# Optimization experiments

Measured on AMD Instinct MI355X. Metric: run time of the kernel, lower is better.

Reference implementation:

```python
import jax, jax.numpy as jnp
import numpy as np

B, T = 256, 50
N_ITEMS = 100000
EMB = 256      # embedding
KBD = 128      # KBembedding == MN_dims
HID = 256      # layers[0] == layers[-1]
OUT = 256      # out_dim
NF = 10        # MN_nfactors == n_r


def setup_inputs() -> dict:
    key = jax.random.key(0)
    ks = jax.random.split(key, 18)
    s = 0.05
    return {
        "X": jax.random.randint(ks[0], (B, T), 0, N_ITEMS),
        "E": jax.random.normal(ks[1], (N_ITEMS, EMB), jnp.float32) * s,
        "KBE": jax.random.normal(ks[2], (N_ITEMS, KBD), jnp.float32) * s,
        "r_matrix": jax.random.normal(ks[3], (NF, KBD), jnp.float32) * s,
        "W_ih": jax.random.normal(ks[4], (3 * HID, EMB), jnp.float32) * s,
        "W_hh": jax.random.normal(ks[5], (3 * HID, HID), jnp.float32) * s,
        "b_ih": jnp.zeros((3 * HID,), jnp.float32),
        "b_hh": jnp.zeros((3 * HID,), jnp.float32),
        "MNu_W": jax.random.normal(ks[6], (KBD, HID), jnp.float32) * s,
        "MNu_b": jnp.zeros((KBD,), jnp.float32),
        "MNu2_W": jax.random.normal(ks[7], (HID, KBD + HID), jnp.float32) * s,
        "MNu2_b": jnp.zeros((HID,), jnp.float32),
        "MNea_W": jax.random.normal(ks[8], (KBD, KBD), jnp.float32) * s,
        "MNea_b": jnp.zeros((KBD,), jnp.float32),
        "mlp1_W": jax.random.normal(ks[9], (OUT, HID), jnp.float32) * s,
        "mlp1_b": jnp.zeros((OUT,), jnp.float32),
        "mlp2_W": jax.random.normal(ks[10], (OUT, EMB + KBD), jnp.float32) * s,
        "mlp2_b": jnp.zeros((OUT,), jnp.float32),
    }


def _gru_cell(x, h, W_ih, W_hh, b_ih, b_hh):
    # PyTorch GRUCell: gates stacked [r, z, n] along dim 0 of weights
    gi = x @ W_ih.T + b_ih
    gh = h @ W_hh.T + b_hh
    ir, iz, inn = jnp.split(gi, 3, axis=-1)
    hr, hz, hn = jnp.split(gh, 3, axis=-1)
    r = jax.nn.sigmoid(ir + hr)
    z = jax.nn.sigmoid(iz + hz)
    n = jnp.tanh(inn + r * hn)
    return (1.0 - z) * n + z * h


def reference(X, E, KBE, r_matrix, W_ih, W_hh, b_ih, b_hh,
              MNu_W, MNu_b, MNu2_W, MNu2_b, MNea_W, MNea_b,
              mlp1_W, mlp1_b, mlp2_W, mlp2_b):
    Bv, Tv = X.shape
    Em = E.at[0].set(0.0)     # mask row 0 of E
    KBm = KBE.at[0].set(0.0)  # mask row 0 of KBE
    Sx = Em[X]                # (B, T, EMB)
    KBItem = KBm[X]           # (B, T, KBD)

    def step(carry, xs):
        h, MN, y_sum = carry
        x_t, kb_t = xs                      # (B, EMB), (B, KBD)
        h = _gru_cell(x_t, h, W_ih, W_hh, b_ih, b_hh)
        y = h                                # dropout p=0 -> identity
        # gated memory write
        EA = jnp.tanh(kb_t @ MNea_W.T + MNea_b)          # (B, KBD)
        EA = EA[:, None, :] + r_matrix                    # (B, NF, KBD)
        gate = jax.nn.sigmoid(jnp.sum(MN * EA, axis=-1, keepdims=True))  # (B, NF, 1)
        MN = MN * (1.0 - gate) + EA * gate
        # attention read
        U = jnp.tanh(y @ MNu_W.T + MNu_b)                 # (B, KBD)
        AW = jax.nn.softmax(U @ r_matrix.T, axis=1)       # (B, NF)
        AC = jnp.einsum('bfd,bf->bd', MN, AW)             # (B, KBD)
        Ut = jnp.tanh(jnp.concatenate([y, AC], axis=-1) @ MNu2_W.T + MNu2_b)  # (B, HID)
        y_out = jnp.tanh(Ut @ mlp1_W.T + mlp1_b)          # (B, OUT)
        return (h, MN, y_sum + y_out), None

    init = (jnp.zeros((Bv, HID), Sx.dtype),
            jnp.zeros((Bv, NF, KBD), Sx.dtype),
            jnp.zeros((Bv, OUT), Sx.dtype))
    xs = (jnp.swapaxes(Sx, 0, 1), jnp.swapaxes(KBItem, 0, 1))  # (T, B, *)
    (h, MN, y_sum), _ = jax.lax.scan(step, init, xs)
    y = y_sum / Tv

    MergeE = jnp.concatenate([E, KBE], axis=1).at[0].set(0.0)  # (N, EMB+KBD)
    Sy = jnp.tanh(MergeE @ mlp2_W.T + mlp2_b)                  # (N, OUT)
    scores = jax.nn.log_softmax(y @ Sy.T, axis=1)              # (B, N)
    return scores, y
```

## Files before the change

kernel.cpp:

```cpp
#include <hip/hip_runtime.h>

typedef _Float16 f16;
typedef _Float16 f16x4 __attribute__((ext_vector_type(4)));
typedef _Float16 f16x8 __attribute__((ext_vector_type(8)));
typedef float f32x4 __attribute__((ext_vector_type(4)));

#define MFMA16(a,b,c) __builtin_amdgcn_mfma_f32_16x16x32_f16(a,b,c,0,0,0)

#define NITEMS 100000
#define NBLK4  1563

#define OFF_WIH   0u
#define OFF_WHH   393216u
#define OFF_MNU   786432u
#define OFF_MNU2  851968u
#define OFF_MNEA  1048576u
#define OFF_MLP1  1081344u
#define OFF_MLP2  1212416u
#define OFF_GI    1409024u
#define OFF_TV    21069824u
#define OFF_MN    24346624u
#define OFF_YALL  57114624u
#define OFF_SY    66945024u
#define OFF_Y16   118407168u
#define OFF_PMAX  118538240u
#define OFF_PSUM  120176640u
#define OFF_LSE   121815040u

__device__ __forceinline__ float sigm(float x) { return 1.f / (1.f + __expf(-x)); }
__device__ __forceinline__ float tanh_fast(float x) {
  return 1.f - 2.f / (1.f + __expf(2.f * x));
}

__global__ __launch_bounds__(256) void k_pack(
    const float* s0, const float* s1, const float* s2, const float* s3,
    const float* s4, const float* s5, const float* s6, f16* base)
{
  int fid = blockIdx.x * 256 + threadIdx.x;
  const float* src; f16* dst; int K, f;
  if (fid < 24576)      { src = s0; dst = base;          K = 256; f = fid; }
  else if (fid < 49152) { src = s1; dst = base + 196608; K = 256; f = fid - 24576; }
  else if (fid < 53248) { src = s2; dst = base + 393216; K = 256; f = fid - 49152; }
  else if (fid < 65536) { src = s3; dst = base + 425984; K = 384; f = fid - 53248; }
  else if (fid < 67584) { src = s4; dst = base + 524288; K = 128; f = fid - 65536; }
  else if (fid < 75776) { src = s5; dst = base + 540672; K = 256; f = fid - 67584; }
  else                  { src = s6; dst = base + 606208; K = 384; f = fid - 75776; }
  int lane = f & 63, t2 = f >> 6, KS = K >> 5;
  int ks = t2 % KS, nt = t2 / KS;
  int row = nt * 16 + (lane & 15), col = ks * 32 + ((lane >> 4) << 3);
  const float* sp = src + (size_t)row * K + col;
  f16x8 v;
  #pragma unroll
  for (int j = 0; j < 8; j++) v[j] = (f16)sp[j];
  *(f16x8*)(dst + (size_t)f * 8) = v;
}

__global__ __launch_bounds__(512) void k_giea(
    const int* __restrict__ X, const float* __restrict__ E,
    const f16* __restrict__ Wih_p, const float* __restrict__ bih,
    const float* __restrict__ bhh, f16* __restrict__ gi2,
    const float* __restrict__ KBE, const f16* __restrict__ Wea_p,
    const float* __restrict__ bea, f16* __restrict__ tv)
{
  __shared__ __align__(16) char smem[66048];
  f16 (*At)[264] = (f16(*)[264])smem;
  f16* Lg2 = (f16*)(smem + 16896);
  int tid = threadIdx.x;
  int w = tid >> 6, lane = tid & 63, lr = lane & 15, lg = lane >> 4;
  if (blockIdx.x < 400) {
    int r0g = blockIdx.x * 32;
    int t = r0g >> 8;
    int grp0 = (r0g & 255) >> 3;
    {
      int r = tid >> 4, c = (tid & 15) * 16;
      int b = (r0g + r) & 255;
      int item = X[b * 50 + t];
      if (item == 0) {
        #pragma unroll
        for (int j = 0; j < 16; j++) At[r][c + j] = (f16)0.f;
      } else {
        const float4* sp = (const float4*)(E + (size_t)item * 256 + c);
        #pragma unroll
        for (int q = 0; q < 4; q++) {
          float4 v = sp[q];
          At[r][c + q*4 + 0] = (f16)v.x; At[r][c + q*4 + 1] = (f16)v.y;
          At[r][c + q*4 + 2] = (f16)v.z; At[r][c + q*4 + 3] = (f16)v.w;
        }
      }
    }
    __syncthreads();
    f32x4 acc[2][6] = {};
    for (int ks = 0; ks < 8; ks++) {
      f16x8 a0 = *(const f16x8*)(&At[lr][ks * 32 + lg * 8]);
      f16x8 a1 = *(const f16x8*)(&At[16 + lr][ks * 32 + lg * 8]);
      #pragma unroll
      for (int j = 0; j < 6; j++) {
        int nt = w * 6 + j;
        f16x8 bf = *(const f16x8*)(Wih_p + ((size_t)((nt * 8 + ks) * 64 + lane) << 3));
        acc[0][j] = MFMA16(a0, bf, acc[0][j]);
        acc[1][j] = MFMA16(a1, bf, acc[1][j]);
      }
    }
    int lane_s = ((lg & 1) << 4) | lr;
    #pragma unroll
    for (int j = 0; j < 6; j++) {
      int tile = w * 6 + j;
      int gate = tile >> 4, w_s = tile & 15;
      int col = tile * 16 + lr;
      float bias = bih[col] + (col < 512 ? bhh[col] : 0.f);
      #pragma unroll
      for (int mt = 0; mt < 2; mt++) {
        int grp_local = mt * 2 + (lg >> 1);
        f16* dstp = Lg2 + (((grp_local * 16 + w_s) * 32 + lane_s) * 12 + gate * 4);
        #pragma unroll
        for (int rr = 0; rr < 4; rr++)
          dstp[rr] = (f16)(acc[mt][j][rr] + bias);
      }
    }
    __syncthreads();
    f16* dst = gi2 + ((size_t)t * 32 + grp0) * 6144;
    #pragma unroll
    for (int q = 0; q < 6; q++) {
      int i = q * 512 + tid;
      *(f16x8*)(dst + i * 8) = *(const f16x8*)(Lg2 + i * 8);
    }
  } else {
    int r0 = (blockIdx.x - 400) * 32;
    int t = r0 >> 8;
    {
      int r = tid >> 4, c = (tid & 15) * 8;
      int b = (r0 + r) & 255;
      int item = X[b * 50 + t];
      if (item == 0) {
        #pragma unroll
        for (int j = 0; j < 8; j++) At[r][c + j] = (f16)0.f;
      } else {
        const float4* sp = (const float4*)(KBE + (size_t)item * 128 + c);
        #pragma unroll
        for (int q = 0; q < 2; q++) {
          float4 v = sp[q];
          At[r][c + q*4 + 0] = (f16)v.x; At[r][c + q*4 + 1] = (f16)v.y;
          At[r][c + q*4 + 2] = (f16)v.z; At[r][c + q*4 + 3] = (f16)v.w;
        }
      }
    }
    __syncthreads();
    f32x4 acc[2] = {};
    for (int ks = 0; ks < 4; ks++) {
      f16x8 a0 = *(const f16x8*)(&At[lr][ks * 32 + lg * 8]);
      f16x8 a1 = *(const f16x8*)(&At[16 + lr][ks * 32 + lg * 8]);
      f16x8 bf = *(const f16x8*)(Wea_p + ((size_t)((w * 4 + ks) * 64 + lane) << 3));
      acc[0] = MFMA16(a0, bf, acc[0]);
      acc[1] = MFMA16(a1, bf, acc[1]);
    }
    f16* tvs = Lg2;
    int col = w * 16 + lr;
    float bias = bea[col];
    #pragma unroll
    for (int mt = 0; mt < 2; mt++)
      #pragma unroll
      for (int rr = 0; rr < 4; rr++)
        tvs[(mt * 16 + lg * 4 + rr) * 128 + col] = (f16)tanh_fast(acc[mt][rr] + bias);
    __syncthreads();
    {
      int row = tid >> 4, c = (tid & 15) * 8;
      *(f16x8*)(tv + (size_t)(r0 + row) * 128 + c) = *(const f16x8*)(tvs + row * 128 + c);
    }
  }
}

__global__ __launch_bounds__(1024)
__attribute__((amdgpu_waves_per_eu(4, 4)))
void k_fused(
    const f16* __restrict__ Whh_p, const float* __restrict__ bhh,
    const f16* __restrict__ gi2, f16* __restrict__ y_all,
    const f16* __restrict__ tv, const float* __restrict__ Rm, f16* __restrict__ MN,
    const float* __restrict__ E, const float* __restrict__ KBE,
    const f16* __restrict__ mlp2_p, const float* __restrict__ mlp2b, f16* __restrict__ Sy)
{
  __shared__ __align__(16) char smem[147456];
  int tid = threadIdx.x, w = tid >> 6, lane = tid & 63, lr = lane & 15, lg = lane >> 4;

  if (blockIdx.x < 32) {
    f16* Wlds = (f16*)smem;
    f16* hb0 = (f16*)(smem + 131072);
    f16* hb1 = (f16*)(smem + 139264);
    int r0 = blockIdx.x * 8;
    {
      const float4* src = (const float4*)Whh_p;
      float4* dst = (float4*)Wlds;
      #pragma unroll
      for (int i = 0; i < 8; i++) dst[tid + i * 1024] = src[tid + i * 1024];
      float4 z4 = {0.f, 0.f, 0.f, 0.f};
      ((float4*)hb0)[tid] = z4;
    }
    int col = w * 16 + lr;
    float bN = bhh[col + 512];
    float hreg[4] = {0.f, 0.f, 0.f, 0.f};
    const f16* gP = gi2 + (size_t)blockIdx.x * 6144 + (size_t)(w * 32 + lane) * 12;
    f16x8 P0 = {};
    f16x4 P1 = {};
    if (lg < 2) {
      P0 = *(const f16x8*)gP;
      P1 = *(const f16x4*)(gP + 8);
    }
    __syncthreads();
    f16* hc = hb0; f16* hn_ = hb1;
    int xr = (lr & 7) << 4;
    const f16* wB0 = Wlds + (size_t)w * 4096 + lane * 8;
    const f16* wBz = Whh_p + ((size_t)((16 + w) * 8) * 64 + lane) * 8;
    const f16* wBn = Whh_p + ((size_t)((32 + w) * 8) * 64 + lane) * 8;
    for (int t = 0; t < 50; t++) {
      f32x4 aR = {}, aZ = {}, aN = {};
      const char* hbase = (const char*)hc + lr * 512;
      #pragma unroll
      for (int ks = 0; ks < 8; ks++) {
        f16x8 a = *(const f16x8*)(hbase + ((ks * 64 + lg * 16) ^ xr));
        aR = MFMA16(a, *(const f16x8*)(wB0 + ks * 512), aR);
        aZ = MFMA16(a, *(const f16x8*)(wBz + ks * 512), aZ);
        aN = MFMA16(a, *(const f16x8*)(wBn + ks * 512), aN);
      }
      if (lg < 2) {
        #pragma unroll
        for (int rr = 0; rr < 4; rr++) {
          int row = lg * 4 + rr;
          float rg = sigm((float)P0[rr] + aR[rr]);
          float zg = sigm((float)P0[4 + rr] + aZ[rr]);
          float ng = tanh_fast((float)P1[rr] + rg * (aN[rr] + bN));
          float hv = ng + zg * (hreg[rr] - ng);
          hreg[rr] = hv;
          *(f16*)((char*)hn_ + row * 512 + ((col * 2) ^ ((row & 7) << 4))) = (f16)hv;
        }
        if (t < 49) {
          const f16* gN = gP + (size_t)(t + 1) * 196608;
          P0 = *(const f16x8*)gN;
          P1 = *(const f16x4*)(gN + 8);
        }
      }
      __syncthreads();
      if (tid < 256) {
        int row = tid >> 5, c = tid & 31;
        f16x8 hv = *(const f16x8*)((char*)hn_ + row * 512 + ((c * 16) ^ ((row & 7) << 4)));
        *(f16x8*)(y_all + ((size_t)t * 256 + r0 + row) * 256 + c * 8) = hv;
      }
      f16* tmp = hc; hc = hn_; hn_ = tmp;
    }
  } else if (blockIdx.x < 192) {
    int pair = (blockIdx.x - 32) * 16 + w;
    int b = pair / 10, f = pair - (pair / 10) * 10;
    float r0_ = Rm[f * 128 + lane], r1_ = Rm[f * 128 + 64 + lane];
    float mn0 = 0.f, mn1 = 0.f;
    float c0 = (float)tv[(size_t)b * 128 + lane];
    float c1 = (float)tv[(size_t)b * 128 + 64 + lane];
    for (int t = 0; t < 50; t++) {
      float ea0 = c0 + r0_;
      float ea1 = c1 + r1_;
      if (t < 49) {
        size_t nb = ((size_t)(t + 1) * 256 + b) * 128;
        c0 = (float)tv[nb + lane];
        c1 = (float)tv[nb + 64 + lane];
      }
      float p = mn0 * ea0 + mn1 * ea1;
      #pragma unroll
      for (int off = 32; off > 0; off >>= 1) p += __shfl_xor(p, off);
      float g = sigm(p);
      mn0 += (ea0 - mn0) * g;
      mn1 += (ea1 - mn1) * g;
      size_t mb = (((size_t)t * 256 + b) * 10 + f) * 128;
      MN[mb + lane] = (f16)mn0;
      MN[mb + 64 + lane] = (f16)mn1;
    }
  } else {
    f16* At = (f16*)smem;
    int i0 = (blockIdx.x - 192) * 32;
    {
      int r = tid >> 5;
      int item = i0 + r;
      int c = (tid & 31) * 8;
      if (item == 0) {
        #pragma unroll
        for (int j = 0; j < 8; j++) At[r * 392 + c + j] = (f16)0.f;
      } else {
        const float4* sp = (const float4*)(E + (size_t)item * 256 + c);
        #pragma unroll
        for (int q = 0; q < 2; q++) {
          float4 v = sp[q];
          At[r * 392 + c + q*4 + 0] = (f16)v.x; At[r * 392 + c + q*4 + 1] = (f16)v.y;
          At[r * 392 + c + q*4 + 2] = (f16)v.z; At[r * 392 + c + q*4 + 3] = (f16)v.w;
        }
      }
      int c2 = (tid & 31) * 4;
      if (item == 0) {
        #pragma unroll
        for (int j = 0; j < 4; j++) At[r * 392 + 256 + c2 + j] = (f16)0.f;
      } else {
        float4 v = *(const float4*)(KBE + (size_t)item * 128 + c2);
        At[r * 392 + 256 + c2 + 0] = (f16)v.x; At[r * 392 + 256 + c2 + 1] = (f16)v.y;
        At[r * 392 + 256 + c2 + 2] = (f16)v.z; At[r * 392 + 256 + c2 + 3] = (f16)v.w;
      }
    }
    __syncthreads();
    int mt = w & 1, ntp = w >> 1;
    f32x4 acc[2] = {};
    for (int ks = 0; ks < 12; ks++) {
      f16x8 a = *(const f16x8*)(&At[(mt * 16 + lr) * 392 + ks * 32 + lg * 8]);
      #pragma unroll
      for (int j = 0; j < 2; j++) {
        int nt = ntp * 2 + j;
        f16x8 bf = *(const f16x8*)(mlp2_p + ((size_t)((nt * 12 + ks) * 64 + lane) << 3));
        acc[j] = MFMA16(a, bf, acc[j]);
      }
    }
    #pragma unroll
    for (int j = 0; j < 2; j++) {
      int col = (ntp * 2 + j) * 16 + lr;
      float bias = mlp2b[col];
      #pragma unroll
      for (int rr = 0; rr < 4; rr++) {
        int item = i0 + mt * 16 + lg * 4 + rr;
        Sy[(size_t)item * 256 + col] = (f16)tanh_fast(acc[j][rr] + bias);
      }
    }
  }
}

__global__ __launch_bounds__(512) void k_uacut(
    const f16* __restrict__ y_all, const f16* __restrict__ MNu_p,
    const float* __restrict__ MNub, const float* __restrict__ Rm,
    const f16* __restrict__ MN,
    const f16* __restrict__ MNu2_p, const float* __restrict__ MNu2b,
    const f16* __restrict__ mlp1_p, const float* __restrict__ mlp1b,
    float* __restrict__ ypart)
{
  __shared__ __align__(16) char smem[25088];
  int tid = threadIdx.x, w = tid >> 6, lane = tid & 63, lr = lane & 15, lg = lane >> 4;
  f16   (*Aty)[264] = (f16(*)[264])smem;
  float (*Uf)[136]  = (float(*)[136])(smem + 8448);
  f16   (*Utl)[264] = (f16(*)[264])(smem + 8448);
  float (*Lg)[10]   = (float(*)[10])(smem + 17152);
  float (*Aw)[10]   = (float(*)[10])(smem + 17792);
  f16   (*ACs)[136] = (f16(*)[136])(smem + 18432);
  int r0 = blockIdx.x * 16;
  {
    int r = tid >> 5, c = (tid & 31) * 8;
    f16x8 v = *(const f16x8*)(y_all + (size_t)(r0 + r) * 256 + c);
    *(f16x8*)(&Aty[r][c]) = v;
  }
  __syncthreads();
  {
    f32x4 acc = {};
    for (int ks = 0; ks < 8; ks++) {
      f16x8 a = *(const f16x8*)(&Aty[lr][ks * 32 + lg * 8]);
      f16x8 bf = *(const f16x8*)(MNu_p + ((size_t)((w * 8 + ks) * 64 + lane) << 3));
      acc = MFMA16(a, bf, acc);
    }
    int col = w * 16 + lr;
    float bias = MNub[col];
    #pragma unroll
    for (int rr = 0; rr < 4; rr++)
      Uf[lg * 4 + rr][col] = tanh_fast(acc[rr] + bias);
  }
  __syncthreads();
  if (tid < 160) {
    int row = tid / 10, f = tid - (tid / 10) * 10;
    float s = 0.f;
    for (int d = 0; d < 128; d++) s += Uf[row][d] * Rm[f * 128 + d];
    Lg[row][f] = s;
  }
  __syncthreads();
  if (tid < 16) {
    float m = -1e30f;
    #pragma unroll
    for (int f = 0; f < 10; f++) m = fmaxf(m, Lg[tid][f]);
    float e[10], s = 0.f;
    #pragma unroll
    for (int f = 0; f < 10; f++) { e[f] = __expf(Lg[tid][f] - m); s += e[f]; }
    float inv = 1.f / s;
    #pragma unroll
    for (int f = 0; f < 10; f++) Aw[tid][f] = e[f] * inv;
  }
  __syncthreads();
  if (tid < 256) {
    int row = tid >> 4, d0 = (tid & 15) * 8;
    float a[8] = {0,0,0,0,0,0,0,0};
    for (int f = 0; f < 10; f++) {
      float wgt = Aw[row][f];
      f16x8 mv = *(const f16x8*)(MN + (((size_t)(r0 + row)) * 10 + f) * 128 + d0);
      #pragma unroll
      for (int q = 0; q < 8; q++) a[q] += wgt * (float)mv[q];
    }
    f16x8 o;
    #pragma unroll
    for (int q = 0; q < 8; q++) o[q] = (f16)a[q];
    *(f16x8*)(&ACs[row][d0]) = o;
  }
  __syncthreads();
  {
    f32x4 acc[2] = {};
    for (int ks = 0; ks < 12; ks++) {
      f16x8 a = (ks < 8)
        ? *(const f16x8*)(&Aty[lr][ks * 32 + lg * 8])
        : *(const f16x8*)(&ACs[lr][(ks - 8) * 32 + lg * 8]);
      #pragma unroll
      for (int j = 0; j < 2; j++) {
        f16x8 bf = *(const f16x8*)(MNu2_p + ((size_t)(((w * 2 + j) * 12 + ks) * 64 + lane) << 3));
        acc[j] = MFMA16(a, bf, acc[j]);
      }
    }
    __syncthreads();
    #pragma unroll
    for (int j = 0; j < 2; j++) {
      int col = (w * 2 + j) * 16 + lr;
      float bias = MNu2b[col];
      #pragma unroll
      for (int rr = 0; rr < 4; rr++)
        Utl[lg * 4 + rr][col] = (f16)tanh_fast(acc[j][rr] + bias);
    }
  }
  __syncthreads();
  {
    f32x4 acc2[2] = {};
    for (int ks = 0; ks < 8; ks++) {
      f16x8 a = *(const f16x8*)(&Utl[lr][ks * 32 + lg * 8]);
      #pragma unroll
      for (int j = 0; j < 2; j++) {
        f16x8 bf = *(const f16x8*)(mlp1_p + ((size_t)(((w * 2 + j) * 8 + ks) * 64 + lane) << 3));
        acc2[j] = MFMA16(a, bf, acc2[j]);
      }
    }
    #pragma unroll
    for (int j = 0; j < 2; j++) {
      int col = (w * 2 + j) * 16 + lr;
      float bias = mlp1b[col];
      #pragma unroll
      for (int rr = 0; rr < 4; rr++) {
        int row = r0 + lg * 4 + rr;
        ypart[(size_t)row * 256 + col] = tanh_fast(acc2[j][rr] + bias);
      }
    }
  }
}

__global__ __launch_bounds__(256) void k_yfin(
    const float* __restrict__ ypart, float* __restrict__ outy, f16* __restrict__ y16)
{
  int b = blockIdx.x, c = threadIdx.x;
  float s = 0.f;
  for (int t = 0; t < 50; t++) s += ypart[((size_t)t * 256 + b) * 256 + c];
  float v = s * (1.0f / 50.0f);
  outy[b * 256 + c] = v;
  y16[b * 256 + c] = (f16)v;
}

__global__ __launch_bounds__(512) void k_score0(
    const f16* __restrict__ y16, const f16* __restrict__ Sy,
    float* __restrict__ pmax, float* __restrict__ psum)
{
  __shared__ float pm[512], ps[512];
  int tid = threadIdx.x, w = tid >> 6, lane = tid & 63, lr = lane & 15, lg = lane >> 4;
  int i0 = blockIdx.x * 64;
  int mtb = (w >> 1) * 4, ntb = (w & 1) * 2;
  f32x4 acc[4][2] = {};
  for (int ks = 0; ks < 8; ks++) {
    f16x8 a[4];
    #pragma unroll
    for (int i = 0; i < 4; i++)
      a[i] = *(const f16x8*)(y16 + ((size_t)((mtb + i) * 16 + lr)) * 256 + ks * 32 + lg * 8);
    #pragma unroll
    for (int j = 0; j < 2; j++) {
      int item = i0 + (ntb + j) * 16 + lr;
      int ic = item < NITEMS ? item : (NITEMS - 1);
      f16x8 bv = *(const f16x8*)(Sy + (size_t)ic * 256 + ks * 32 + lg * 8);
      #pragma unroll
      for (int i = 0; i < 4; i++) acc[i][j] = MFMA16(a[i], bv, acc[i][j]);
    }
  }
  {
    int item0 = i0 + ntb * 16 + lr, item1 = item0 + 16;
    bool v0 = item0 < NITEMS, v1 = item1 < NITEMS;
    #pragma unroll
    for (int i = 0; i < 4; i++)
      #pragma unroll
      for (int rr = 0; rr < 4; rr++) {
        float x0 = v0 ? acc[i][0][rr] : -1e30f;
        float x1 = v1 ? acc[i][1][rr] : -1e30f;
        float m = fmaxf(x0, x1);
        m = fmaxf(m, __shfl_xor(m, 1)); m = fmaxf(m, __shfl_xor(m, 2));
        m = fmaxf(m, __shfl_xor(m, 4)); m = fmaxf(m, __shfl_xor(m, 8));
        float s = (v0 ? __expf(x0 - m) : 0.f) + (v1 ? __expf(x1 - m) : 0.f);
        s += __shfl_xor(s, 1); s += __shfl_xor(s, 2);
        s += __shfl_xor(s, 4); s += __shfl_xor(s, 8);
        if (lr == 0) {
          int row = (mtb + i) * 16 + lg * 4 + rr;
          pm[(w & 1) * 256 + row] = m;
          ps[(w & 1) * 256 + row] = s;
        }
      }
  }
  __syncthreads();
  if (tid < 256) {
    float m0 = pm[tid], m1 = pm[256 + tid];
    float s0 = ps[tid], s1 = ps[256 + tid];
    float M = fmaxf(m0, m1);
    float S = s0 * __expf(m0 - M) + s1 * __expf(m1 - M);
    pmax[(size_t)tid * 1600 + blockIdx.x] = M;
    psum[(size_t)tid * 1600 + blockIdx.x] = S;
  }
}

__global__ __launch_bounds__(256) void k_lse(
    const float* __restrict__ pmax, const float* __restrict__ psum, float* __restrict__ lse)
{
  int b = blockIdx.x, tid = threadIdx.x;
  __shared__ float red[256];
  float m = -1e30f;
  for (int i = tid; i < NBLK4; i += 256) m = fmaxf(m, pmax[(size_t)b * 1600 + i]);
  red[tid] = m; __syncthreads();
  for (int s = 128; s > 0; s >>= 1) {
    if (tid < s) red[tid] = fmaxf(red[tid], red[tid + s]);
    __syncthreads();
  }
  float M = red[0]; __syncthreads();
  float s = 0.f;
  for (int i = tid; i < NBLK4; i += 256)
    s += psum[(size_t)b * 1600 + i] * __expf(pmax[(size_t)b * 1600 + i] - M);
  red[tid] = s; __syncthreads();
  for (int q = 128; q > 0; q >>= 1) {
    if (tid < q) red[tid] += red[tid + q];
    __syncthreads();
  }
  if (tid == 0) lse[b] = M + logf(red[0]);
}

__global__ __launch_bounds__(512) void k_scores1(
    const f16* __restrict__ y16, const f16* __restrict__ Sy,
    const float* __restrict__ lse, float* __restrict__ out)
{
  __shared__ float lse_s[256];
  int tid = threadIdx.x, w = tid >> 6, lane = tid & 63, lr = lane & 15, lg = lane >> 4;
  if (tid < 256) lse_s[tid] = lse[tid];
  int i0 = blockIdx.x * 64;
  int mtb = (w >> 1) * 4, ntb = (w & 1) * 2;
  f32x4 acc[4][2] = {};
  for (int ks = 0; ks < 8; ks++) {
    f16x8 a[4];
    #pragma unroll
    for (int i = 0; i < 4; i++)
      a[i] = *(const f16x8*)(y16 + ((size_t)((mtb + i) * 16 + lr)) * 256 + ks * 32 + lg * 8);
    #pragma unroll
    for (int j = 0; j < 2; j++) {
      int item = i0 + (ntb + j) * 16 + lr;
      int ic = item < NITEMS ? item : (NITEMS - 1);
      f16x8 bv = *(const f16x8*)(Sy + (size_t)ic * 256 + ks * 32 + lg * 8);
      #pragma unroll
      for (int i = 0; i < 4; i++) acc[i][j] = MFMA16(a[i], bv, acc[i][j]);
    }
  }
  __syncthreads();
  #pragma unroll
  for (int i = 0; i < 4; i++)
    #pragma unroll
    for (int j = 0; j < 2; j++) {
      int c = i0 + (ntb + j) * 16 + lr;
      if (c < NITEMS) {
        #pragma unroll
        for (int rr = 0; rr < 4; rr++) {
          int row = (mtb + i) * 16 + lg * 4 + rr;
          out[(size_t)row * NITEMS + c] = acc[i][j][rr] - lse_s[row];
        }
      }
    }
}

extern "C" void kernel_launch(void* const* d_in, const int* in_sizes, int n_in,
                              void* d_out, int out_size, void* d_ws, size_t ws_size,
                              hipStream_t stream) {
  (void)in_sizes; (void)n_in; (void)out_size; (void)ws_size;
  const int*   X     = (const int*)d_in[0];
  const float* E     = (const float*)d_in[1];
  const float* KBE   = (const float*)d_in[2];
  const float* Rm    = (const float*)d_in[3];
  const float* Wih   = (const float*)d_in[4];
  const float* Whh   = (const float*)d_in[5];
  const float* bih   = (const float*)d_in[6];
  const float* bhh   = (const float*)d_in[7];
  const float* MNuW  = (const float*)d_in[8];
  const float* MNub  = (const float*)d_in[9];
  const float* MNu2W = (const float*)d_in[10];
  const float* MNu2b = (const float*)d_in[11];
  const float* MNeaW = (const float*)d_in[12];
  const float* MNeab = (const float*)d_in[13];
  const float* mlp1W = (const float*)d_in[14];
  const float* mlp1b = (const float*)d_in[15];
  const float* mlp2W = (const float*)d_in[16];
  const float* mlp2b = (const float*)d_in[17];

  char* ws = (char*)d_ws;
  f16*   Wih_p  = (f16*)(ws + OFF_WIH);
  f16*   Whh_p  = (f16*)(ws + OFF_WHH);
  f16*   MNu_p  = (f16*)(ws + OFF_MNU);
  f16*   MNu2_p = (f16*)(ws + OFF_MNU2);
  f16*   Wea_p  = (f16*)(ws + OFF_MNEA);
  f16*   mlp1_p = (f16*)(ws + OFF_MLP1);
  f16*   mlp2_p = (f16*)(ws + OFF_MLP2);
  f16*   gi2    = (f16*)(ws + OFF_GI);
  f16*   tv     = (f16*)(ws + OFF_TV);
  f16*   MN     = (f16*)(ws + OFF_MN);
  f16*   y_all  = (f16*)(ws + OFF_YALL);
  f16*   Sy     = (f16*)(ws + OFF_SY);
  float* ypart  = (float*)(ws + OFF_GI);
  f16*   y16    = (f16*)(ws + OFF_Y16);
  float* pmax   = (float*)(ws + OFF_PMAX);
  float* psum   = (float*)(ws + OFF_PSUM);
  float* lse    = (float*)(ws + OFF_LSE);
  float* outf   = (float*)d_out;

  k_pack<<<344, 256, 0, stream>>>(Wih, Whh, MNuW, MNu2W, MNeaW, mlp1W, mlp2W, (f16*)ws);
  k_giea<<<800, 512, 0, stream>>>(X, E, Wih_p, bih, bhh, gi2, KBE, Wea_p, MNeab, tv);
  k_fused<<<3317, 1024, 0, stream>>>(Whh_p, bhh, gi2, y_all, tv, Rm, MN,
                                     E, KBE, mlp2_p, mlp2b, Sy);
  k_uacut<<<800, 512, 0, stream>>>(y_all, MNu_p, MNub, Rm, MN,
                                   MNu2_p, MNu2b, mlp1_p, mlp1b, ypart);
  k_yfin<<<256, 256, 0, stream>>>(ypart, outf + 25600000, y16);
  k_score0<<<NBLK4, 512, 0, stream>>>(y16, Sy, pmax, psum);
  k_lse<<<256, 256, 0, stream>>>(pmax, psum, lse);
  k_scores1<<<NBLK4, 512, 0, stream>>>(y16, Sy, lse, outf);
}
```

Baseline: 368.4 us.

## Run GRU scan one batch row per block with register-resident W_hh dot2

Replaces the 32-block MFMA GRU recurrence, which staged W_hh in LDS and processed 8 batch rows per block, with 256 blocks that each run one batch row. Every block keeps its slice of W_hh in registers and computes the recurrent gates with fdot2 plus cross-lane shuffles. The Sy (mlp2) projection moves out of the fused scan kernel into the prep kernel, and the gi layout becomes a plain row-major layout. The aim is to spread the serial recurrence across more CUs and shorten per-step latency, at the cost of loading W_hh once per block and heavier register use.

```diff
diff --git a/kernel.cpp b/kernel.cpp
--- a/kernel.cpp
+++ b/kernel.cpp
@@ -1,9 +1,10 @@
 #include <hip/hip_runtime.h>
 
 typedef _Float16 f16;
-typedef _Float16 f16x4 __attribute__((ext_vector_type(4)));
+typedef _Float16 f16x2 __attribute__((ext_vector_type(2)));
 typedef _Float16 f16x8 __attribute__((ext_vector_type(8)));
 typedef float f32x4 __attribute__((ext_vector_type(4)));
+typedef int i32x4 __attribute__((ext_vector_type(4)));
 
 #define MFMA16(a,b,c) __builtin_amdgcn_mfma_f32_16x16x32_f16(a,b,c,0,0,0)
 
@@ -17,26 +18,48 @@
 #define OFF_MNEA  1048576u
 #define OFF_MLP1  1081344u
 #define OFF_MLP2  1212416u
-#define OFF_GI    1409024u
-#define OFF_TV    21069824u
-#define OFF_MN    24346624u
-#define OFF_YALL  57114624u
-#define OFF_SY    66945024u
-#define OFF_Y16   118407168u
-#define OFF_PMAX  118538240u
-#define OFF_PSUM  120176640u
-#define OFF_LSE   121815040u
+#define OFF_WHHD  1409024u
+#define OFF_GI    1802240u
+#define OFF_TV    21463040u
+#define OFF_MN    24739840u
+#define OFF_YALL  57507840u
+#define OFF_SY    64061440u
+#define OFF_Y16   115261440u
+#define OFF_PMAX  115392512u
+#define OFF_PSUM  117030912u
+#define OFF_LSE   118669312u
 
 __device__ __forceinline__ float sigm(float x) { return 1.f / (1.f + __expf(-x)); }
 __device__ __forceinline__ float tanh_fast(float x) {
   return 1.f - 2.f / (1.f + __expf(2.f * x));
 }
+__device__ __forceinline__ float fdot2(f16x2 a, f16x2 b, float c) {
+#if defined(__has_builtin)
+#if __has_builtin(__builtin_amdgcn_fdot2)
+  return __builtin_amdgcn_fdot2(a, b, c, false);
+#else
+  return fmaf((float)a[1], (float)b[1], fmaf((float)a[0], (float)b[0], c));
+#endif
+#else
+  return fmaf((float)a[1], (float)b[1], fmaf((float)a[0], (float)b[0], c));
+#endif
+}
 
 __global__ __launch_bounds__(256) void k_pack(
     const float* s0, const float* s1, const float* s2, const float* s3,
     const float* s4, const float* s5, const float* s6, f16* base)
 {
   int fid = blockIdx.x * 256 + threadIdx.x;
+  if (fid >= 88064) {
+    int g = fid - 88064;
+    const float* sp = s1 + (size_t)g * 8;
+    f16* dst = (f16*)((char*)base + OFF_WHHD);
+    f16x8 v;
+    #pragma unroll
+    for (int j = 0; j < 8; j++) v[j] = (f16)sp[j];
+    *(f16x8*)(dst + (size_t)g * 8) = v;
+    return;
+  }
   const float* src; f16* dst; int K, f;
   if (fid < 24576)      { src = s0; dst = base;          K = 256; f = fid; }
   else if (fid < 49152) { src = s1; dst = base + 196608; K = 256; f = fid - 24576; }
@@ -55,12 +78,13 @@
   *(f16x8*)(dst + (size_t)f * 8) = v;
 }
 
-__global__ __launch_bounds__(512) void k_giea(
+__global__ __launch_bounds__(512) void k_prep(
     const int* __restrict__ X, const float* __restrict__ E,
     const f16* __restrict__ Wih_p, const float* __restrict__ bih,
-    const float* __restrict__ bhh, f16* __restrict__ gi2,
+    const float* __restrict__ bhh, f16* __restrict__ gi,
     const float* __restrict__ KBE, const f16* __restrict__ Wea_p,
-    const float* __restrict__ bea, f16* __restrict__ tv)
+    const float* __restrict__ bea, f16* __restrict__ tv,
+    const f16* __restrict__ mlp2_p, const float* __restrict__ mlp2b, f16* __restrict__ Sy)
 {
   __shared__ __align__(16) char smem[66048];
   f16 (*At)[264] = (f16(*)[264])smem;
@@ -70,7 +94,6 @@
   if (blockIdx.x < 400) {
     int r0g = blockIdx.x * 32;
     int t = r0g >> 8;
-    int grp0 = (r0g & 255) >> 3;
     {
       int r = tid >> 4, c = (tid & 15) * 16;
       int b = (r0g + r) & 255;
@@ -101,30 +124,24 @@
         acc[1][j] = MFMA16(a1, bf, acc[1][j]);
       }
     }
-    int lane_s = ((lg & 1) << 4) | lr;
     #pragma unroll
     for (int j = 0; j < 6; j++) {
-      int tile = w * 6 + j;
-      int gate = tile >> 4, w_s = tile & 15;
-      int col = tile * 16 + lr;
+      int col = (w * 6 + j) * 16 + lr;
       float bias = bih[col] + (col < 512 ? bhh[col] : 0.f);
       #pragma unroll
-      for (int mt = 0; mt < 2; mt++) {
-        int grp_local = mt * 2 + (lg >> 1);
-        f16* dstp = Lg2 + (((grp_local * 16 + w_s) * 32 + lane_s) * 12 + gate * 4);
+      for (int mt = 0; mt < 2; mt++)
         #pragma unroll
         for (int rr = 0; rr < 4; rr++)
-          dstp[rr] = (f16)(acc[mt][j][rr] + bias);
-      }
-    }
-    __syncthreads();
-    f16* dst = gi2 + ((size_t)t * 32 + grp0) * 6144;
+          Lg2[(mt * 16 + lg * 4 + rr) * 768 + col] = (f16)(acc[mt][j][rr] + bias);
+    }
+    __syncthreads();
+    f16* dst = gi + (size_t)r0g * 768;
     #pragma unroll
     for (int q = 0; q < 6; q++) {
-      int i = q * 512 + tid;
-      *(f16x8*)(dst + i * 8) = *(const f16x8*)(Lg2 + i * 8);
-    }
-  } else {
+      int u = q * 512 + tid;
+      *(f16x8*)(dst + u * 8) = *(const f16x8*)(Lg2 + u * 8);
+    }
+  } else if (blockIdx.x < 800) {
     int r0 = (blockIdx.x - 400) * 32;
     int t = r0 >> 8;
     {
@@ -166,87 +183,132 @@
       int row = tid >> 4, c = (tid & 15) * 8;
       *(f16x8*)(tv + (size_t)(r0 + row) * 128 + c) = *(const f16x8*)(tvs + row * 128 + c);
     }
-  }
-}
-
-__global__ __launch_bounds__(1024)
-__attribute__((amdgpu_waves_per_eu(4, 4)))
-void k_fused(
-    const f16* __restrict__ Whh_p, const float* __restrict__ bhh,
-    const f16* __restrict__ gi2, f16* __restrict__ y_all,
-    const f16* __restrict__ tv, const float* __restrict__ Rm, f16* __restrict__ MN,
-    const float* __restrict__ E, const float* __restrict__ KBE,
-    const f16* __restrict__ mlp2_p, const float* __restrict__ mlp2b, f16* __restrict__ Sy)
-{
-  __shared__ __align__(16) char smem[147456];
-  int tid = threadIdx.x, w = tid >> 6, lane = tid & 63, lr = lane & 15, lg = lane >> 4;
-
-  if (blockIdx.x < 32) {
-    f16* Wlds = (f16*)smem;
-    f16* hb0 = (f16*)(smem + 131072);
-    f16* hb1 = (f16*)(smem + 139264);
-    int r0 = blockIdx.x * 8;
+  } else {
+    f16* A2 = (f16*)smem;
+    int i0 = (blockIdx.x - 800) * 32;
     {
-      const float4* src = (const float4*)Whh_p;
-      float4* dst = (float4*)Wlds;
-      #pragma unroll
-      for (int i = 0; i < 8; i++) dst[tid + i * 1024] = src[tid + i * 1024];
-      float4 z4 = {0.f, 0.f, 0.f, 0.f};
-      ((float4*)hb0)[tid] = z4;
-    }
-    int col = w * 16 + lr;
-    float bN = bhh[col + 512];
-    float hreg[4] = {0.f, 0.f, 0.f, 0.f};
-    const f16* gP = gi2 + (size_t)blockIdx.x * 6144 + (size_t)(w * 32 + lane) * 12;
-    f16x8 P0 = {};
-    f16x4 P1 = {};
-    if (lg < 2) {
-      P0 = *(const f16x8*)gP;
-      P1 = *(const f16x4*)(gP + 8);
-    }
-    __syncthreads();
-    f16* hc = hb0; f16* hn_ = hb1;
-    int xr = (lr & 7) << 4;
-    const f16* wB0 = Wlds + (size_t)w * 4096 + lane * 8;
-    const f16* wBz = Whh_p + ((size_t)((16 + w) * 8) * 64 + lane) * 8;
-    const f16* wBn = Whh_p + ((size_t)((32 + w) * 8) * 64 + lane) * 8;
+      int r = tid >> 4;
+      int item = i0 + r;
+      f16* rowp = A2 + r * 392;
+      int cE = (tid & 15) * 16, cK = (tid & 15) * 8;
+      if (item == 0) {
+        #pragma unroll
+        for (int j = 0; j < 16; j++) rowp[cE + j] = (f16)0.f;
+        #pragma unroll
+        for (int j = 0; j < 8; j++) rowp[256 + cK + j] = (f16)0.f;
+      } else {
+        const float4* sp = (const float4*)(E + (size_t)item * 256 + cE);
+        #pragma unroll
+        for (int q = 0; q < 4; q++) {
+          float4 v = sp[q];
+          rowp[cE + q*4 + 0] = (f16)v.x; rowp[cE + q*4 + 1] = (f16)v.y;
+          rowp[cE + q*4 + 2] = (f16)v.z; rowp[cE + q*4 + 3] = (f16)v.w;
+        }
+        const float4* kp = (const float4*)(KBE + (size_t)item * 128 + cK);
+        #pragma unroll
+        for (int q = 0; q < 2; q++) {
+          float4 v = kp[q];
+          rowp[256 + cK + q*4 + 0] = (f16)v.x; rowp[256 + cK + q*4 + 1] = (f16)v.y;
+          rowp[256 + cK + q*4 + 2] = (f16)v.z; rowp[256 + cK + q*4 + 3] = (f16)v.w;
+        }
+      }
+    }
+    __syncthreads();
+    int mt = w & 1, nq = w >> 1;
+    f32x4 acc[4] = {};
+    for (int ks = 0; ks < 12; ks++) {
+      f16x8 a = *(const f16x8*)(&A2[(mt * 16 + lr) * 392 + ks * 32 + lg * 8]);
+      #pragma unroll
+      for (int j = 0; j < 4; j++) {
+        int nt = nq * 4 + j;
+        f16x8 bf = *(const f16x8*)(mlp2_p + ((size_t)((nt * 12 + ks) * 64 + lane) << 3));
+        acc[j] = MFMA16(a, bf, acc[j]);
+      }
+    }
+    #pragma unroll
+    for (int j = 0; j < 4; j++) {
+      int col = (nq * 4 + j) * 16 + lr;
+      float bias = mlp2b[col];
+      #pragma unroll
+      for (int rr = 0; rr < 4; rr++) {
+        int item = i0 + mt * 16 + lg * 4 + rr;
+        Sy[(size_t)item * 256 + col] = (f16)tanh_fast(acc[j][rr] + bias);
+      }
+    }
+  }
+}
+
+__global__ __launch_bounds__(1024) void k_scan(
+    const f16* __restrict__ Whh_d, const float* __restrict__ bhh,
+    const f16* __restrict__ gi, f16* __restrict__ y_all,
+    const f16* __restrict__ tv, const float* __restrict__ Rm, f16* __restrict__ MN)
+{
+  int tid = threadIdx.x, w = tid >> 6, l = tid & 63;
+  if (blockIdx.x < 256) {
+    __shared__ __align__(16) f16 hbuf[4 * 72];
+    __shared__ float ghbuf[768];
+    int b = blockIdx.x;
+    int chunk = l >> 4, cl = l & 15;
+    i32x4 Wv[3][8];
+    #pragma unroll
+    for (int j = 0; j < 3; j++) {
+      int col = w * 48 + j * 16 + cl;
+      const f16* wp = Whh_d + (size_t)col * 256 + chunk * 64;
+      #pragma unroll
+      for (int m = 0; m < 8; m++)
+        Wv[j][m] = *(const i32x4*)(wp + m * 8);
+    }
+    float hprev = 0.f, bN = 0.f;
+    f16 gr = (f16)0.f, gz = (f16)0.f, gn = (f16)0.f;
+    if (tid < 256) {
+      hbuf[(tid >> 6) * 72 + (tid & 63)] = (f16)0.f;
+      bN = bhh[512 + tid];
+      const f16* g0 = gi + (size_t)b * 768 + tid;
+      gr = g0[0]; gz = g0[256]; gn = g0[512];
+    }
+    __syncthreads();
+    const f16* hb = hbuf + chunk * 72;
     for (int t = 0; t < 50; t++) {
-      f32x4 aR = {}, aZ = {}, aN = {};
-      const char* hbase = (const char*)hc + lr * 512;
-      #pragma unroll
-      for (int ks = 0; ks < 8; ks++) {
-        f16x8 a = *(const f16x8*)(hbase + ((ks * 64 + lg * 16) ^ xr));
-        aR = MFMA16(a, *(const f16x8*)(wB0 + ks * 512), aR);
-        aZ = MFMA16(a, *(const f16x8*)(wBz + ks * 512), aZ);
-        aN = MFMA16(a, *(const f16x8*)(wBn + ks * 512), aN);
-      }
-      if (lg < 2) {
-        #pragma unroll
-        for (int rr = 0; rr < 4; rr++) {
-          int row = lg * 4 + rr;
-          float rg = sigm((float)P0[rr] + aR[rr]);
-          float zg = sigm((float)P0[4 + rr] + aZ[rr]);
-          float ng = tanh_fast((float)P1[rr] + rg * (aN[rr] + bN));
-          float hv = ng + zg * (hreg[rr] - ng);
-          hreg[rr] = hv;
-          *(f16*)((char*)hn_ + row * 512 + ((col * 2) ^ ((row & 7) << 4))) = (f16)hv;
-        }
-        if (t < 49) {
-          const f16* gN = gP + (size_t)(t + 1) * 196608;
-          P0 = *(const f16x8*)gN;
-          P1 = *(const f16x4*)(gN + 8);
-        }
+      float s0 = 0.f, s1 = 0.f, s2 = 0.f;
+      #pragma unroll
+      for (int m = 0; m < 8; m++) {
+        i32x4 hw = *(const i32x4*)(hb + m * 8);
+        #pragma unroll
+        for (int p = 0; p < 4; p++) {
+          f16x2 hp = __builtin_bit_cast(f16x2, hw[p]);
+          s0 = fdot2(hp, __builtin_bit_cast(f16x2, Wv[0][m][p]), s0);
+          s1 = fdot2(hp, __builtin_bit_cast(f16x2, Wv[1][m][p]), s1);
+          s2 = fdot2(hp, __builtin_bit_cast(f16x2, Wv[2][m][p]), s2);
+        }
+      }
+      s0 += __shfl_xor(s0, 16); s0 += __shfl_xor(s0, 32);
+      s1 += __shfl_xor(s1, 16); s1 += __shfl_xor(s1, 32);
+      s2 += __shfl_xor(s2, 16); s2 += __shfl_xor(s2, 32);
+      if (l < 16) {
+        ghbuf[w * 48 + l]      = s0;
+        ghbuf[w * 48 + 16 + l] = s1;
+        ghbuf[w * 48 + 32 + l] = s2;
       }
       __syncthreads();
       if (tid < 256) {
-        int row = tid >> 5, c = tid & 31;
-        f16x8 hv = *(const f16x8*)((char*)hn_ + row * 512 + ((c * 16) ^ ((row & 7) << 4)));
-        *(f16x8*)(y_all + ((size_t)t * 256 + r0 + row) * 256 + c * 8) = hv;
-      }
-      f16* tmp = hc; hc = hn_; hn_ = tmp;
-    }
-  } else if (blockIdx.x < 192) {
-    int pair = (blockIdx.x - 32) * 16 + w;
+        int c = tid;
+        float rg = sigm((float)gr + ghbuf[c]);
+        float zg = sigm((float)gz + ghbuf[256 + c]);
+        float ng = tanh_fast((float)gn + rg * (ghbuf[512 + c] + bN));
+        float hv = ng + zg * (hprev - ng);
+        hprev = hv;
+        hbuf[(c >> 6) * 72 + (c & 63)] = (f16)hv;
+        y_all[((size_t)t * 256 + b) * 256 + c] = (f16)hv;
+        if (t < 49) {
+          const f16* gN = gi + ((size_t)(t + 1) * 256 + b) * 768 + c;
+          gr = gN[0]; gz = gN[256]; gn = gN[512];
+        }
+      }
+      __syncthreads();
+    }
+  } else {
+    int lane = l;
+    int pair = (blockIdx.x - 256) * 16 + w;
     int b = pair / 10, f = pair - (pair / 10) * 10;
     float r0_ = Rm[f * 128 + lane], r1_ = Rm[f * 128 + 64 + lane];
     float mn0 = 0.f, mn1 = 0.f;
@@ -269,57 +331,6 @@
       size_t mb = (((size_t)t * 256 + b) * 10 + f) * 128;
       MN[mb + lane] = (f16)mn0;
       MN[mb + 64 + lane] = (f16)mn1;
-    }
-  } else {
-    f16* At = (f16*)smem;
-    int i0 = (blockIdx.x - 192) * 32;
-    {
-      int r = tid >> 5;
-      int item = i0 + r;
-      int c = (tid & 31) * 8;
-      if (item == 0) {
-        #pragma unroll
-        for (int j = 0; j < 8; j++) At[r * 392 + c + j] = (f16)0.f;
-      } else {
-        const float4* sp = (const float4*)(E + (size_t)item * 256 + c);
-        #pragma unroll
-        for (int q = 0; q < 2; q++) {
-          float4 v = sp[q];
-          At[r * 392 + c + q*4 + 0] = (f16)v.x; At[r * 392 + c + q*4 + 1] = (f16)v.y;
-          At[r * 392 + c + q*4 + 2] = (f16)v.z; At[r * 392 + c + q*4 + 3] = (f16)v.w;
-        }
-      }
-      int c2 = (tid & 31) * 4;
-      if (item == 0) {
-        #pragma unroll
-        for (int j = 0; j < 4; j++) At[r * 392 + 256 + c2 + j] = (f16)0.f;
-      } else {
-        float4 v = *(const float4*)(KBE + (size_t)item * 128 + c2);
-        At[r * 392 + 256 + c2 + 0] = (f16)v.x; At[r * 392 + 256 + c2 + 1] = (f16)v.y;
-        At[r * 392 + 256 + c2 + 2] = (f16)v.z; At[r * 392 + 256 + c2 + 3] = (f16)v.w;
-      }
-    }
-    __syncthreads();
-    int mt = w & 1, ntp = w >> 1;
-    f32x4 acc[2] = {};
-    for (int ks = 0; ks < 12; ks++) {
-      f16x8 a = *(const f16x8*)(&At[(mt * 16 + lr) * 392 + ks * 32 + lg * 8]);
-      #pragma unroll
-      for (int j = 0; j < 2; j++) {
-        int nt = ntp * 2 + j;
-        f16x8 bf = *(const f16x8*)(mlp2_p + ((size_t)((nt * 12 + ks) * 64 + lane) << 3));
-        acc[j] = MFMA16(a, bf, acc[j]);
-      }
-    }
-    #pragma unroll
-    for (int j = 0; j < 2; j++) {
-      int col = (ntp * 2 + j) * 16 + lr;
-      float bias = mlp2b[col];
-      #pragma unroll
-      for (int rr = 0; rr < 4; rr++) {
-        int item = i0 + mt * 16 + lg * 4 + rr;
-        Sy[(size_t)item * 256 + col] = (f16)tanh_fast(acc[j][rr] + bias);
-      }
     }
   }
 }
@@ -597,13 +608,13 @@
 
   char* ws = (char*)d_ws;
   f16*   Wih_p  = (f16*)(ws + OFF_WIH);
-  f16*   Whh_p  = (f16*)(ws + OFF_WHH);
   f16*   MNu_p  = (f16*)(ws + OFF_MNU);
   f16*   MNu2_p = (f16*)(ws + OFF_MNU2);
   f16*   Wea_p  = (f16*)(ws + OFF_MNEA);
   f16*   mlp1_p = (f16*)(ws + OFF_MLP1);
   f16*   mlp2_p = (f16*)(ws + OFF_MLP2);
-  f16*   gi2    = (f16*)(ws + OFF_GI);
+  f16*   Whh_d  = (f16*)(ws + OFF_WHHD);
+  f16*   gi     = (f16*)(ws + OFF_GI);
   f16*   tv     = (f16*)(ws + OFF_TV);
   f16*   MN     = (f16*)(ws + OFF_MN);
   f16*   y_all  = (f16*)(ws + OFF_YALL);
@@ -615,10 +626,10 @@
   float* lse    = (float*)(ws + OFF_LSE);
   float* outf   = (float*)d_out;
 
-  k_pack<<<344, 256, 0, stream>>>(Wih, Whh, MNuW, MNu2W, MNeaW, mlp1W, mlp2W, (f16*)ws);
-  k_giea<<<800, 512, 0, stream>>>(X, E, Wih_p, bih, bhh, gi2, KBE, Wea_p, MNeab, tv);
-  k_fused<<<3317, 1024, 0, stream>>>(Whh_p, bhh, gi2, y_all, tv, Rm, MN,
-                                     E, KBE, mlp2_p, mlp2b, Sy);
+  k_pack<<<440, 256, 0, stream>>>(Wih, Whh, MNuW, MNu2W, MNeaW, mlp1W, mlp2W, (f16*)ws);
+  k_prep<<<3925, 512, 0, stream>>>(X, E, Wih_p, bih, bhh, gi, KBE, Wea_p, MNeab, tv,
+                                   mlp2_p, mlp2b, Sy);
+  k_scan<<<416, 1024, 0, stream>>>(Whh_d, bhh, gi, y_all, tv, Rm, MN);
   k_uacut<<<800, 512, 0, stream>>>(y_all, MNu_p, MNub, Rm, MN,
                                    MNu2_p, MNu2b, mlp1_p, mlp1b, ypart);
   k_yfin<<<256, 256, 0, stream>>>(ypart, outf + 25600000, y16);
```

After: 398.6 us. 8.2% more time.

## Store raw f16 logits in first scoring pass and replace GEMM recompute with elementwise fix

Applied to the files above, without the earlier changes.

The first scoring pass now also writes the raw logits as f16 into a reused workspace region. The second pass, which recomputed the whole y·Syᵀ GEMM, is replaced by a simple elementwise kernel that reads those logits, subtracts the per-row log-sum-exp and writes float4-coalesced outputs. This trades the repeated read of Sy and the repeated MFMA work for an extra 51 MB f16 write and read. It also adds f16 rounding error to the final log-softmax scores.

```diff
diff --git a/kernel.cpp b/kernel.cpp
--- a/kernel.cpp
+++ b/kernel.cpp
@@ -452,9 +452,9 @@
   y16[b * 256 + c] = (f16)v;
 }
 
-__global__ __launch_bounds__(512) void k_score0(
+__global__ __launch_bounds__(512) void k_scoreraw(
     const f16* __restrict__ y16, const f16* __restrict__ Sy,
-    float* __restrict__ pmax, float* __restrict__ psum)
+    float* __restrict__ pmax, float* __restrict__ psum, f16* __restrict__ raw)
 {
   __shared__ float pm[512], ps[512];
   int tid = threadIdx.x, w = tid >> 6, lane = tid & 63, lr = lane & 15, lg = lane >> 4;
@@ -475,6 +475,19 @@
       for (int i = 0; i < 4; i++) acc[i][j] = MFMA16(a[i], bv, acc[i][j]);
     }
   }
+  #pragma unroll
+  for (int i = 0; i < 4; i++)
+    #pragma unroll
+    for (int j = 0; j < 2; j++) {
+      int c = i0 + (ntb + j) * 16 + lr;
+      if (c < NITEMS) {
+        #pragma unroll
+        for (int rr = 0; rr < 4; rr++) {
+          int row = (mtb + i) * 16 + lg * 4 + rr;
+          raw[(size_t)row * NITEMS + c] = (f16)acc[i][j][rr];
+        }
+      }
+    }
   {
     int item0 = i0 + ntb * 16 + lr, item1 = item0 + 16;
     bool v0 = item0 < NITEMS, v1 = item1 < NITEMS;
@@ -532,44 +545,22 @@
   if (tid == 0) lse[b] = M + logf(red[0]);
 }
 
-__global__ __launch_bounds__(512) void k_scores1(
-    const f16* __restrict__ y16, const f16* __restrict__ Sy,
-    const float* __restrict__ lse, float* __restrict__ out)
-{
-  __shared__ float lse_s[256];
-  int tid = threadIdx.x, w = tid >> 6, lane = tid & 63, lr = lane & 15, lg = lane >> 4;
-  if (tid < 256) lse_s[tid] = lse[tid];
-  int i0 = blockIdx.x * 64;
-  int mtb = (w >> 1) * 4, ntb = (w & 1) * 2;
-  f32x4 acc[4][2] = {};
-  for (int ks = 0; ks < 8; ks++) {
-    f16x8 a[4];
-    #pragma unroll
-    for (int i = 0; i < 4; i++)
-      a[i] = *(const f16x8*)(y16 + ((size_t)((mtb + i) * 16 + lr)) * 256 + ks * 32 + lg * 8);
-    #pragma unroll
-    for (int j = 0; j < 2; j++) {
-      int item = i0 + (ntb + j) * 16 + lr;
-      int ic = item < NITEMS ? item : (NITEMS - 1);
-      f16x8 bv = *(const f16x8*)(Sy + (size_t)ic * 256 + ks * 32 + lg * 8);
-      #pragma unroll
-      for (int i = 0; i < 4; i++) acc[i][j] = MFMA16(a[i], bv, acc[i][j]);
-    }
-  }
-  __syncthreads();
-  #pragma unroll
-  for (int i = 0; i < 4; i++)
-    #pragma unroll
-    for (int j = 0; j < 2; j++) {
-      int c = i0 + (ntb + j) * 16 + lr;
-      if (c < NITEMS) {
-        #pragma unroll
-        for (int rr = 0; rr < 4; rr++) {
-          int row = (mtb + i) * 16 + lg * 4 + rr;
-          out[(size_t)row * NITEMS + c] = acc[i][j][rr] - lse_s[row];
-        }
-      }
-    }
+__global__ __launch_bounds__(256) void k_fix(
+    const f16* __restrict__ raw, const float* __restrict__ lse, float* __restrict__ out)
+{
+  int row = blockIdx.y;
+  int idx = blockIdx.x * 256 + threadIdx.x;
+  if (idx < 12500) {
+    float l = lse[row];
+    f16x8 v = *(const f16x8*)(raw + (size_t)row * NITEMS + idx * 8);
+    float4 o0, o1;
+    o0.x = (float)v[0] - l; o0.y = (float)v[1] - l;
+    o0.z = (float)v[2] - l; o0.w = (float)v[3] - l;
+    o1.x = (float)v[4] - l; o1.y = (float)v[5] - l;
+    o1.z = (float)v[6] - l; o1.w = (float)v[7] - l;
+    float4* p = (float4*)(out + (size_t)row * NITEMS + idx * 8);
+    p[0] = o0; p[1] = o1;
+  }
 }
 
 extern "C" void kernel_launch(void* const* d_in, const int* in_sizes, int n_in,
@@ -609,6 +600,7 @@
   f16*   y_all  = (f16*)(ws + OFF_YALL);
   f16*   Sy     = (f16*)(ws + OFF_SY);
   float* ypart  = (float*)(ws + OFF_GI);
+  f16*   raw    = (f16*)(ws + OFF_GI);
   f16*   y16    = (f16*)(ws + OFF_Y16);
   float* pmax   = (float*)(ws + OFF_PMAX);
   float* psum   = (float*)(ws + OFF_PSUM);
@@ -622,7 +614,8 @@
   k_uacut<<<800, 512, 0, stream>>>(y_all, MNu_p, MNub, Rm, MN,
                                    MNu2_p, MNu2b, mlp1_p, mlp1b, ypart);
   k_yfin<<<256, 256, 0, stream>>>(ypart, outf + 25600000, y16);
-  k_score0<<<NBLK4, 512, 0, stream>>>(y16, Sy, pmax, psum);
+  k_scoreraw<<<NBLK4, 512, 0, stream>>>(y16, Sy, pmax, psum, raw);
   k_lse<<<256, 256, 0, stream>>>(pmax, psum, lse);
-  k_scores1<<<NBLK4, 512, 0, stream>>>(y16, Sy, lse, outf);
-}
+  dim3 gfix(49, 256);
+  k_fix<<<gfix, 256, 0, stream>>>(raw, lse, outf);
+}
```

Result: faster. 319.9 us (median of 2 runs) (-13.2%).
